# Performance work log

Hardware: AMD Instinct MI355X
Metric: run time of the kernel (lower is better)

## Reference

```python
import jax, jax.numpy as jnp
import numpy as np

GROUP_SIZE = 128
SCALE_MIN = 1e-8
IN_FEATURES = 4096
OUT_FEATURES = 4096
BATCH, SEQ = 4, 2048


def quantize_literati(weight, scales):
    """w -> sign(w) * clamp(scale) per group of GROUP_SIZE along last dim.
    in_features is divisible by GROUP_SIZE, so no padding branch is needed.
    """
    O, C = weight.shape
    wg = weight.reshape(O, C // GROUP_SIZE, GROUP_SIZE)
    # torch.sign with zeros mapped to +1
    signs = jnp.where(wg >= 0, 1.0, -1.0).astype(weight.dtype)
    s = jnp.maximum(scales, SCALE_MIN)  # (O, num_groups)
    w_q = signs * s[..., None]
    return w_q.reshape(O, C)


def setup_inputs() -> dict:
    key = jax.random.key(0)
    kx, kw = jax.random.split(key)
    x = jax.random.normal(kx, (BATCH, SEQ, IN_FEATURES), dtype=jnp.float32)
    # kaiming_uniform_(a=sqrt(5)) -> U(-1/sqrt(fan_in), 1/sqrt(fan_in))
    bound = 1.0 / np.sqrt(IN_FEATURES)
    weight = jax.random.uniform(kw, (OUT_FEATURES, IN_FEATURES), dtype=jnp.float32,
                                minval=-bound, maxval=bound)
    scales = jnp.full((OUT_FEATURES, IN_FEATURES // GROUP_SIZE), 0.1, dtype=jnp.float32)
    return {"x": x, "weight": weight, "scales": scales}


def reference(x, weight, scales):
    w_q = quantize_literati(weight, scales)
    # F.linear: x @ w_q.T
    return jnp.einsum('bsc,oc->bso', x, w_q)
```

## Files before the change

### kernel.cpp

```cpp
#include <hip/hip_runtime.h>
#include <hip/hip_bf16.h>
#include <stdint.h>
#include <stddef.h>


#define M_DIM 8192
#define N_DIM 4096
#define K_DIM 4096
#define BM 128
#define BN 128
#define BK 64

typedef __bf16 bf16x8 __attribute__((ext_vector_type(8)));
typedef __bf16 bf16x4 __attribute__((ext_vector_type(4)));
typedef float f32x4 __attribute__((ext_vector_type(4)));

__device__ __forceinline__ void async_copy16(const void* g, void* l) {
  __builtin_amdgcn_global_load_lds((__attribute__((address_space(1))) void*)g,
                                   (__attribute__((address_space(3))) void*)l,
                                   16, 0, 0);
}

__global__ void cast_x_kernel(const float* __restrict__ in, __bf16* __restrict__ out) {
  const int i = blockIdx.x * blockDim.x + threadIdx.x;
  const float4 v = ((const float4*)in)[i];
  bf16x4 q;
  q.x = (__bf16)v.x; q.y = (__bf16)v.y; q.z = (__bf16)v.z; q.w = (__bf16)v.w;
  ((bf16x4*)out)[i] = q;
}

__global__ void quant_w_kernel(const float* __restrict__ w,
                               const float* __restrict__ scales,
                               __bf16* __restrict__ out) {
  const int i = blockIdx.x * blockDim.x + threadIdx.x;
  const int idx = i << 2;
  const int o = idx >> 12;
  const int grp = (idx & 4095) >> 7;
  const float s = fmaxf(scales[(o << 5) + grp], 1e-8f);
  const float4 v = ((const float4*)w)[i];
  bf16x4 q;
  q.x = (__bf16)((v.x >= 0.0f) ? s : -s);
  q.y = (__bf16)((v.y >= 0.0f) ? s : -s);
  q.z = (__bf16)((v.z >= 0.0f) ? s : -s);
  q.w = (__bf16)((v.w >= 0.0f) ? s : -s);
  ((bf16x4*)out)[i] = q;
}

template <bool PRECONV>
__global__ __launch_bounds__(256) void literati_gemm(
    const __bf16* __restrict__ Ab, const __bf16* __restrict__ Bb,
    const float* __restrict__ Af, const float* __restrict__ Bf,
    const float* __restrict__ scales, float* __restrict__ C) {
  __shared__ __align__(16) __bf16 As[BM * BK];
  __shared__ __align__(16) __bf16 Bs[BN * BK];

  const int tid = threadIdx.x;
  const int lane = tid & 63;
  const int wave = tid >> 6;
  const int bn0 = blockIdx.x * BN;
  const int bm0 = blockIdx.y * BM;
  const int wm = (wave >> 1) * 64;
  const int wn = (wave & 1) * 64;

  const int l3 = lane >> 3;
  const int l7 = lane & 7;
  const int kc_sw = l7 ^ l3;

  const int q = lane >> 4;
  const int mr = lane & 15;
  const int mx = mr & 7;

  const f32x4 zero = {0.f, 0.f, 0.f, 0.f};
  f32x4 acc[4][4];
#pragma unroll
  for (int i = 0; i < 4; ++i)
#pragma unroll
    for (int j = 0; j < 4; ++j) acc[i][j] = zero;

  for (int k0 = 0; k0 < K_DIM; k0 += BK) {
    if constexpr (PRECONV) {
#pragma unroll
      for (int i = 0; i < 4; ++i) {
        const int c = wave * 4 + i;
        const int row = c * 8 + l3;
        async_copy16(Ab + (size_t)(bm0 + row) * K_DIM + k0 + kc_sw * 8,
                     &As[(c * 64 + lane) * 8]);
      }
#pragma unroll
      for (int i = 0; i < 4; ++i) {
        const int c = wave * 4 + i;
        const int row = c * 8 + l3;
        async_copy16(Bb + (size_t)(bn0 + row) * K_DIM + k0 + kc_sw * 8,
                     &Bs[(c * 64 + lane) * 8]);
      }
      asm volatile("s_waitcnt vmcnt(0)" ::: "memory");
    } else {
#pragma unroll
      for (int i = 0; i < 4; ++i) {
        const int c = wave * 4 + i;
        const int row = c * 8 + l3;
        const float* src = Af + (size_t)(bm0 + row) * K_DIM + k0 + kc_sw * 8;
        const float4 v0 = ((const float4*)src)[0];
        const float4 v1 = ((const float4*)src)[1];
        bf16x8 o;
        o[0] = (__bf16)v0.x; o[1] = (__bf16)v0.y;
        o[2] = (__bf16)v0.z; o[3] = (__bf16)v0.w;
        o[4] = (__bf16)v1.x; o[5] = (__bf16)v1.y;
        o[6] = (__bf16)v1.z; o[7] = (__bf16)v1.w;
        *(bf16x8*)&As[(c * 64 + lane) * 8] = o;
      }
#pragma unroll
      for (int i = 0; i < 4; ++i) {
        const int c = wave * 4 + i;
        const int row = c * 8 + l3;
        const int gr = bn0 + row;
        const float* src = Bf + (size_t)gr * K_DIM + k0 + kc_sw * 8;
        const float s = fmaxf(scales[(gr << 5) + ((k0 + kc_sw * 8) >> 7)], 1e-8f);
        const float4 v0 = ((const float4*)src)[0];
        const float4 v1 = ((const float4*)src)[1];
        bf16x8 o;
        o[0] = (__bf16)((v0.x >= 0.f) ? s : -s);
        o[1] = (__bf16)((v0.y >= 0.f) ? s : -s);
        o[2] = (__bf16)((v0.z >= 0.f) ? s : -s);
        o[3] = (__bf16)((v0.w >= 0.f) ? s : -s);
        o[4] = (__bf16)((v1.x >= 0.f) ? s : -s);
        o[5] = (__bf16)((v1.y >= 0.f) ? s : -s);
        o[6] = (__bf16)((v1.z >= 0.f) ? s : -s);
        o[7] = (__bf16)((v1.w >= 0.f) ? s : -s);
        *(bf16x8*)&Bs[(c * 64 + lane) * 8] = o;
      }
    }
    __syncthreads();

#pragma unroll
    for (int ks = 0; ks < 2; ++ks) {
      bf16x8 av[4], bv[4];
#pragma unroll
      for (int i = 0; i < 4; ++i) {
        const int slot = (wm + i * 16 + mr) * 8 + ((ks * 4 + q) ^ mx);
        av[i] = *(const bf16x8*)&As[slot * 8];
      }
#pragma unroll
      for (int j = 0; j < 4; ++j) {
        const int slot = (wn + j * 16 + mr) * 8 + ((ks * 4 + q) ^ mx);
        bv[j] = *(const bf16x8*)&Bs[slot * 8];
      }
#pragma unroll
      for (int i = 0; i < 4; ++i)
#pragma unroll
        for (int j = 0; j < 4; ++j)
          acc[i][j] = __builtin_amdgcn_mfma_f32_16x16x32_bf16(av[i], bv[j],
                                                              acc[i][j], 0, 0, 0);
    }
    __syncthreads();
  }

  const int row0 = q * 4;
#pragma unroll
  for (int i = 0; i < 4; ++i) {
#pragma unroll
    for (int j = 0; j < 4; ++j) {
      const size_t base =
          (size_t)(bm0 + wm + i * 16 + row0) * N_DIM + (bn0 + wn + j * 16 + mr);
#pragma unroll
      for (int r = 0; r < 4; ++r) C[base + (size_t)r * N_DIM] = acc[i][j][r];
    }
  }
}

extern "C" void kernel_launch(void* const* d_in, const int* in_sizes, int n_in,
                              void* d_out, int out_size, void* d_ws, size_t ws_size,
                              hipStream_t stream) {
  const float* x = (const float*)d_in[0];
  const float* w = (const float*)d_in[1];
  const float* sc = (const float*)d_in[2];
  float* out = (float*)d_out;

  const size_t need = ((size_t)M_DIM + (size_t)N_DIM) * K_DIM * sizeof(__bf16);
  dim3 grid(N_DIM / BN, M_DIM / BM);

  if (ws_size >= need) {
    __bf16* xb = (__bf16*)d_ws;
    __bf16* wb = xb + (size_t)M_DIM * K_DIM;
    cast_x_kernel<<<(M_DIM * K_DIM / 4) / 256, 256, 0, stream>>>(x, xb);
    quant_w_kernel<<<(N_DIM * K_DIM / 4) / 256, 256, 0, stream>>>(w, sc, wb);
    literati_gemm<true><<<grid, 256, 0, stream>>>(xb, wb, nullptr, nullptr,
                                                  nullptr, out);
  } else {
    literati_gemm<false><<<grid, 256, 0, stream>>>(nullptr, nullptr, x, w, sc,
                                                   out);
  }
}
```

Baseline: 596.3 us.

## Switch GEMM to 32x32x16 MFMA and merge prep kernels into one launch

Replaces the 16x16x32 bf16 MFMA tiling (4x4 accumulators per wave) with 32x32x16 MFMA (2x2 f32x16 accumulators) and rewrites the LDS fragment indexing and epilogue row mapping to match. This aims to cut LDS fragment reads and instruction overhead per FLOP by using the larger matrix instruction. Separately, it fuses the x cast and weight quantization kernels into a single prep kernel in which each thread handles 16 elements, which removes one launch and widens per-thread work. The epilogue stores now follow the 32x32 output layout, which may change how well the global writes coalesce.

```diff
diff --git a/kernel.cpp b/kernel.cpp
--- a/kernel.cpp
+++ b/kernel.cpp
@@ -12,8 +12,7 @@
 #define BK 64
 
 typedef __bf16 bf16x8 __attribute__((ext_vector_type(8)));
-typedef __bf16 bf16x4 __attribute__((ext_vector_type(4)));
-typedef float f32x4 __attribute__((ext_vector_type(4)));
+typedef float f32x16 __attribute__((ext_vector_type(16)));
 
 __device__ __forceinline__ void async_copy16(const void* g, void* l) {
   __builtin_amdgcn_global_load_lds((__attribute__((address_space(1))) void*)g,
@@ -21,29 +20,51 @@
                                    16, 0, 0);
 }
 
-__global__ void cast_x_kernel(const float* __restrict__ in, __bf16* __restrict__ out) {
-  const int i = blockIdx.x * blockDim.x + threadIdx.x;
-  const float4 v = ((const float4*)in)[i];
-  bf16x4 q;
-  q.x = (__bf16)v.x; q.y = (__bf16)v.y; q.z = (__bf16)v.z; q.w = (__bf16)v.w;
-  ((bf16x4*)out)[i] = q;
-}
-
-__global__ void quant_w_kernel(const float* __restrict__ w,
-                               const float* __restrict__ scales,
-                               __bf16* __restrict__ out) {
-  const int i = blockIdx.x * blockDim.x + threadIdx.x;
-  const int idx = i << 2;
-  const int o = idx >> 12;
-  const int grp = (idx & 4095) >> 7;
-  const float s = fmaxf(scales[(o << 5) + grp], 1e-8f);
-  const float4 v = ((const float4*)w)[i];
-  bf16x4 q;
-  q.x = (__bf16)((v.x >= 0.0f) ? s : -s);
-  q.y = (__bf16)((v.y >= 0.0f) ? s : -s);
-  q.z = (__bf16)((v.z >= 0.0f) ? s : -s);
-  q.w = (__bf16)((v.w >= 0.0f) ? s : -s);
-  ((bf16x4*)out)[i] = q;
+#define X_THREADS ((size_t)M_DIM * K_DIM / 16)
+#define W_THREADS ((size_t)N_DIM * K_DIM / 16)
+__global__ __launch_bounds__(256) void prep_kernel(
+    const float* __restrict__ x, const float* __restrict__ w,
+    const float* __restrict__ scales, __bf16* __restrict__ xb,
+    __bf16* __restrict__ wb) {
+  const size_t t = (size_t)blockIdx.x * blockDim.x + threadIdx.x;
+  if (t < X_THREADS) {
+    const float4* src = (const float4*)x + t * 4;
+    bf16x8* dst = (bf16x8*)xb + t * 2;
+#pragma unroll
+    for (int h = 0; h < 2; ++h) {
+      const float4 v0 = src[h * 2 + 0];
+      const float4 v1 = src[h * 2 + 1];
+      bf16x8 o;
+      o[0] = (__bf16)v0.x; o[1] = (__bf16)v0.y;
+      o[2] = (__bf16)v0.z; o[3] = (__bf16)v0.w;
+      o[4] = (__bf16)v1.x; o[5] = (__bf16)v1.y;
+      o[6] = (__bf16)v1.z; o[7] = (__bf16)v1.w;
+      dst[h] = o;
+    }
+  } else {
+    const size_t u = t - X_THREADS;
+    const size_t idx = u * 16;
+    const int o_ = (int)(idx >> 12);
+    const int grp = (int)(idx & 4095) >> 7;
+    const float s = fmaxf(scales[(o_ << 5) + grp], 1e-8f);
+    const float4* src = (const float4*)w + u * 4;
+    bf16x8* dst = (bf16x8*)wb + u * 2;
+#pragma unroll
+    for (int h = 0; h < 2; ++h) {
+      const float4 v0 = src[h * 2 + 0];
+      const float4 v1 = src[h * 2 + 1];
+      bf16x8 q;
+      q[0] = (__bf16)((v0.x >= 0.f) ? s : -s);
+      q[1] = (__bf16)((v0.y >= 0.f) ? s : -s);
+      q[2] = (__bf16)((v0.z >= 0.f) ? s : -s);
+      q[3] = (__bf16)((v0.w >= 0.f) ? s : -s);
+      q[4] = (__bf16)((v1.x >= 0.f) ? s : -s);
+      q[5] = (__bf16)((v1.y >= 0.f) ? s : -s);
+      q[6] = (__bf16)((v1.z >= 0.f) ? s : -s);
+      q[7] = (__bf16)((v1.w >= 0.f) ? s : -s);
+      dst[h] = q;
+    }
+  }
 }
 
 template <bool PRECONV>
@@ -66,16 +87,17 @@
   const int l7 = lane & 7;
   const int kc_sw = l7 ^ l3;
 
-  const int q = lane >> 4;
-  const int mr = lane & 15;
-  const int mx = mr & 7;
-
-  const f32x4 zero = {0.f, 0.f, 0.f, 0.f};
-  f32x4 acc[4][4];
-#pragma unroll
-  for (int i = 0; i < 4; ++i)
-#pragma unroll
-    for (int j = 0; j < 4; ++j) acc[i][j] = zero;
+  const int m32 = lane & 31;
+  const int hl = lane >> 5;
+  const int mx7 = m32 & 7;
+
+  f32x16 acc[2][2];
+#pragma unroll
+  for (int i = 0; i < 2; ++i)
+#pragma unroll
+    for (int j = 0; j < 2; ++j)
+#pragma unroll
+      for (int r = 0; r < 16; ++r) acc[i][j][r] = 0.f;
 
   for (int k0 = 0; k0 < K_DIM; k0 += BK) {
     if constexpr (PRECONV) {
@@ -133,37 +155,40 @@
     __syncthreads();
 
 #pragma unroll
-    for (int ks = 0; ks < 2; ++ks) {
-      bf16x8 av[4], bv[4];
-#pragma unroll
-      for (int i = 0; i < 4; ++i) {
-        const int slot = (wm + i * 16 + mr) * 8 + ((ks * 4 + q) ^ mx);
+    for (int ks = 0; ks < 4; ++ks) {
+      bf16x8 av[2], bv[2];
+      const int kc = ks * 2 + hl;
+#pragma unroll
+      for (int i = 0; i < 2; ++i) {
+        const int slot = (wm + i * 32 + m32) * 8 + (kc ^ mx7);
         av[i] = *(const bf16x8*)&As[slot * 8];
       }
 #pragma unroll
-      for (int j = 0; j < 4; ++j) {
-        const int slot = (wn + j * 16 + mr) * 8 + ((ks * 4 + q) ^ mx);
+      for (int j = 0; j < 2; ++j) {
+        const int slot = (wn + j * 32 + m32) * 8 + (kc ^ mx7);
         bv[j] = *(const bf16x8*)&Bs[slot * 8];
       }
 #pragma unroll
-      for (int i = 0; i < 4; ++i)
-#pragma unroll
-        for (int j = 0; j < 4; ++j)
-          acc[i][j] = __builtin_amdgcn_mfma_f32_16x16x32_bf16(av[i], bv[j],
+      for (int i = 0; i < 2; ++i)
+#pragma unroll
+        for (int j = 0; j < 2; ++j)
+          acc[i][j] = __builtin_amdgcn_mfma_f32_32x32x16_bf16(av[i], bv[j],
                                                               acc[i][j], 0, 0, 0);
     }
     __syncthreads();
   }
 
-  const int row0 = q * 4;
-#pragma unroll
-  for (int i = 0; i < 4; ++i) {
-#pragma unroll
-    for (int j = 0; j < 4; ++j) {
-      const size_t base =
-          (size_t)(bm0 + wm + i * 16 + row0) * N_DIM + (bn0 + wn + j * 16 + mr);
-#pragma unroll
-      for (int r = 0; r < 4; ++r) C[base + (size_t)r * N_DIM] = acc[i][j][r];
+#pragma unroll
+  for (int i = 0; i < 2; ++i) {
+#pragma unroll
+    for (int j = 0; j < 2; ++j) {
+      const int col = bn0 + wn + j * 32 + m32;
+      const int rbase = bm0 + wm + i * 32 + 4 * hl;
+#pragma unroll
+      for (int r = 0; r < 16; ++r) {
+        const int row = rbase + (r & 3) + 8 * (r >> 2);
+        C[(size_t)row * N_DIM + col] = acc[i][j][r];
+      }
     }
   }
 }
@@ -182,8 +207,8 @@
   if (ws_size >= need) {
     __bf16* xb = (__bf16*)d_ws;
     __bf16* wb = xb + (size_t)M_DIM * K_DIM;
-    cast_x_kernel<<<(M_DIM * K_DIM / 4) / 256, 256, 0, stream>>>(x, xb);
-    quant_w_kernel<<<(N_DIM * K_DIM / 4) / 256, 256, 0, stream>>>(w, sc, wb);
+    const size_t total_threads = X_THREADS + W_THREADS;
+    prep_kernel<<<(int)(total_threads / 256), 256, 0, stream>>>(x, w, sc, xb, wb);
     literati_gemm<true><<<grid, 256, 0, stream>>>(xb, wb, nullptr, nullptr,
                                                   nullptr, out);
   } else {
```

After: 527.7 us. 1.13x faster.
